# Performance work log

Hardware: AMD Instinct MI355X
Metric: run time of the kernel (lower is better)

The kernel has to match this reference:

```python
import jax, jax.numpy as jnp
from jax import lax
import numpy as np

D_MODEL = 256
EXPAND = 2
D_INNER = D_MODEL * EXPAND
B, T = 8, 4096


def setup_inputs() -> dict:
    key = jax.random.key(0)
    ks = jax.random.split(key, 7)
    s_lin = 1.0 / np.sqrt(D_MODEL)
    s_gru_i = 1.0 / np.sqrt(D_MODEL)  # torch GRU init: U(-1/sqrt(hidden), 1/sqrt(hidden))
    x = jax.random.normal(ks[0], (B, T, D_MODEL), dtype=jnp.float32)
    W1 = jax.random.uniform(ks[1], (D_INNER, D_MODEL), jnp.float32, -s_lin, s_lin)
    b1 = jax.random.uniform(ks[2], (D_INNER,), jnp.float32, -s_lin, s_lin)
    W_ih = jax.random.uniform(ks[3], (3 * D_MODEL, D_INNER), jnp.float32, -s_gru_i, s_gru_i)
    b_ih = jax.random.uniform(ks[4], (3 * D_MODEL,), jnp.float32, -s_gru_i, s_gru_i)
    W_hh = jax.random.uniform(ks[5], (3 * D_MODEL, D_MODEL), jnp.float32, -s_gru_i, s_gru_i)
    b_hh = jax.random.uniform(ks[6], (3 * D_MODEL,), jnp.float32, -s_gru_i, s_gru_i)
    return {"x": x, "W1": W1, "b1": b1, "W_ih": W_ih, "b_ih": b_ih, "W_hh": W_hh, "b_hh": b_hh}


def reference(x, W1, b1, W_ih, b_ih, W_hh, b_hh):
    # Linear(d_model -> d_inner) + exact GELU (torch default)
    h = jax.nn.gelu(jnp.einsum('btd,id->bti', x, W1) + b1, approximate=False)  # [B,T,Di]
    Bb, Tt, _ = h.shape
    H = W_hh.shape[1]
    # Precompute input-side gate pre-activations for all timesteps (order: r, z, n)
    gx = jnp.einsum('bti,gi->btg', h, W_ih) + b_ih  # [B,T,3H]
    gx = jnp.moveaxis(gx, 1, 0)                     # [T,B,3H]

    def step(hprev, g):
        gh = hprev @ W_hh.T + b_hh                  # [B,3H]
        xr, xz, xn = jnp.split(g, 3, axis=-1)
        hr, hz, hn = jnp.split(gh, 3, axis=-1)
        r = jax.nn.sigmoid(xr + hr)
        z = jax.nn.sigmoid(xz + hz)
        n = jnp.tanh(xn + r * hn)
        hnew = (1.0 - z) * n + z * hprev
        return hnew, hnew

    h0 = jnp.zeros((Bb, H), dtype=x.dtype)
    _, out = lax.scan(step, h0, gx)                 # out: [T,B,H]
    return jnp.moveaxis(out, 0, 1)                  # [B,T,H]
```

## Files before the change

### kernel.cpp

```cpp
#include <hip/hip_runtime.h>
#include <hip/hip_fp16.h>
#include <hip/hip_bf16.h>

#define DM   256
#define DI   512
#define TG   768
#define TSEQ 4096
#define NB   8
#define MTOT (NB*TSEQ)

typedef _Float16 h2f __attribute__((ext_vector_type(2)));
typedef _Float16 h8f __attribute__((ext_vector_type(8)));

template<bool A_HALF, bool GELU_ACT>
__global__ __launch_bounds__(256) void gemm_bias(
    const void* __restrict__ Ap, const float* __restrict__ W,
    const float* __restrict__ bias, __half* __restrict__ C,
    int M, int N, int K)
{
  __shared__ float As[16][132];
  __shared__ float Ws[16][132];
  const int tid = threadIdx.x;
  const int tx = tid & 15, ty = tid >> 4;
  const int m0 = blockIdx.y * 128;
  const int n0 = blockIdx.x * 128;

  float acc[8][8] = {};

  for (int k0 = 0; k0 < K; k0 += 16) {
    if constexpr (A_HALF) {
      const __half* A = (const __half*)Ap;
      int r = tid >> 1, seg = (tid & 1) * 8;
      float4 raw = *(const float4*)(A + (size_t)(m0 + r) * K + k0 + seg);
      const __half* hv = (const __half*)&raw;
      #pragma unroll
      for (int q = 0; q < 8; q++) As[seg + q][r] = __half2float(hv[q]);
    } else {
      const float* A = (const float*)Ap;
      #pragma unroll
      for (int rep = 0; rep < 2; rep++) {
        int r = (tid >> 2) + rep * 64;
        int seg = (tid & 3) * 4;
        float4 v = *(const float4*)(A + (size_t)(m0 + r) * K + k0 + seg);
        As[seg + 0][r] = v.x; As[seg + 1][r] = v.y;
        As[seg + 2][r] = v.z; As[seg + 3][r] = v.w;
      }
    }
    #pragma unroll
    for (int rep = 0; rep < 2; rep++) {
      int r = (tid >> 2) + rep * 64;
      int seg = (tid & 3) * 4;
      float4 v = *(const float4*)(W + (size_t)(n0 + r) * K + k0 + seg);
      Ws[seg + 0][r] = v.x; Ws[seg + 1][r] = v.y;
      Ws[seg + 2][r] = v.z; Ws[seg + 3][r] = v.w;
    }
    __syncthreads();
    #pragma unroll
    for (int kk = 0; kk < 16; ++kk) {
      float a[8], b[8];
      *(float4*)&a[0] = *(const float4*)&As[kk][ty * 8];
      *(float4*)&a[4] = *(const float4*)&As[kk][ty * 8 + 4];
      *(float4*)&b[0] = *(const float4*)&Ws[kk][tx * 8];
      *(float4*)&b[4] = *(const float4*)&Ws[kk][tx * 8 + 4];
      #pragma unroll
      for (int i = 0; i < 8; i++)
        #pragma unroll
        for (int j = 0; j < 8; j++)
          acc[i][j] += a[i] * b[j];
    }
    __syncthreads();
  }

  #pragma unroll
  for (int i = 0; i < 8; i++) {
    int m = m0 + ty * 8 + i;
    #pragma unroll
    for (int j = 0; j < 8; j++) {
      int n = n0 + tx * 8 + j;
      float v = acc[i][j] + bias[n];
      if constexpr (GELU_ACT) {
        v = 0.5f * v * (1.0f + erff(v * 0.70710678118654752f));
      }
      C[(size_t)m * N + n] = __float2half(v);
    }
  }
}

__device__ __forceinline__ float dpp_xor1_add(float v) {
  int i = __builtin_bit_cast(int, v);
  int s = __builtin_amdgcn_update_dpp(i, i, 0xB1, 0xF, 0xF, true);
  return v + __builtin_bit_cast(float, s);
}

__global__ __launch_bounds__(512, 2) void gru_scan(
    const __half* __restrict__ gx,
    const float*  __restrict__ Whh,
    const float*  __restrict__ bhh,
    float* __restrict__ out)
{
  const int b = blockIdx.x;
  const int j = threadIdx.x;
  const int u = j >> 1;
  const int p = j & 1;

  __shared__ __align__(16) _Float16 hbuf[2][DM];

  h2f wr[64], wz[64], wn[64];
  {
    const float* rr = Whh + (size_t)u * DM + p * 128;
    const float* rz = rr + (size_t)DM * DM;
    const float* rn = rz + (size_t)DM * DM;
    #pragma unroll
    for (int i = 0; i < 32; ++i) {
      float4 f = *(const float4*)(rr + 4 * i);
      h2f t0; t0[0] = (_Float16)f.x; t0[1] = (_Float16)f.y;
      h2f t1; t1[0] = (_Float16)f.z; t1[1] = (_Float16)f.w;
      wr[2 * i] = t0; wr[2 * i + 1] = t1;
      if (i & 1) __builtin_amdgcn_sched_barrier(0);
    }
    #pragma unroll
    for (int i = 0; i < 32; ++i) {
      float4 f = *(const float4*)(rz + 4 * i);
      h2f t0; t0[0] = (_Float16)f.x; t0[1] = (_Float16)f.y;
      h2f t1; t1[0] = (_Float16)f.z; t1[1] = (_Float16)f.w;
      wz[2 * i] = t0; wz[2 * i + 1] = t1;
      if (i & 1) __builtin_amdgcn_sched_barrier(0);
    }
    #pragma unroll
    for (int i = 0; i < 32; ++i) {
      float4 f = *(const float4*)(rn + 4 * i);
      h2f t0; t0[0] = (_Float16)f.x; t0[1] = (_Float16)f.y;
      h2f t1; t1[0] = (_Float16)f.z; t1[1] = (_Float16)f.w;
      wn[2 * i] = t0; wn[2 * i + 1] = t1;
      if (i & 1) __builtin_amdgcn_sched_barrier(0);
    }
  }
  const float br = bhh[u];
  const float bz = bhh[DM + u];
  const float bn = bhh[2 * DM + u];
  float hloc = 0.0f;

  if (j < DM) hbuf[0][j] = (_Float16)0.0f;
  __syncthreads();

  const __half* gp = gx + (size_t)b * TSEQ * TG;
  float* outb = out + (size_t)b * TSEQ * DM;

  float gxr = __half2float(gp[u]);
  float gxz = __half2float(gp[DM + u]);
  float gxn = __half2float(gp[2 * DM + u]);

  for (int t = 0; t < TSEQ; ++t) {
    const int cur = t & 1;
    const h8f* hp = (const h8f*)(&hbuf[cur][0]) + p * 16;

    float nr = 0.f, nz = 0.f, nn = 0.f;
    if (t + 1 < TSEQ) {
      const __half* g1 = gp + TG;
      nr = __half2float(g1[u]);
      nz = __half2float(g1[DM + u]);
      nn = __half2float(g1[2 * DM + u]);
    }

    float ar = 0.f, az = 0.f, an = 0.f;
    #pragma unroll
    for (int i = 0; i < 16; ++i) {
      union { h8f v; h2f c[4]; } hh;
      hh.v = hp[i];
      ar = __builtin_amdgcn_fdot2(wr[4 * i + 0], hh.c[0], ar, false);
      az = __builtin_amdgcn_fdot2(wz[4 * i + 0], hh.c[0], az, false);
      an = __builtin_amdgcn_fdot2(wn[4 * i + 0], hh.c[0], an, false);
      ar = __builtin_amdgcn_fdot2(wr[4 * i + 1], hh.c[1], ar, false);
      az = __builtin_amdgcn_fdot2(wz[4 * i + 1], hh.c[1], az, false);
      an = __builtin_amdgcn_fdot2(wn[4 * i + 1], hh.c[1], an, false);
      ar = __builtin_amdgcn_fdot2(wr[4 * i + 2], hh.c[2], ar, false);
      az = __builtin_amdgcn_fdot2(wz[4 * i + 2], hh.c[2], az, false);
      an = __builtin_amdgcn_fdot2(wn[4 * i + 2], hh.c[2], an, false);
      ar = __builtin_amdgcn_fdot2(wr[4 * i + 3], hh.c[3], ar, false);
      az = __builtin_amdgcn_fdot2(wz[4 * i + 3], hh.c[3], az, false);
      an = __builtin_amdgcn_fdot2(wn[4 * i + 3], hh.c[3], an, false);
      if (i & 1) __builtin_amdgcn_sched_barrier(0);
    }
    ar = dpp_xor1_add(ar);
    az = dpp_xor1_add(az);
    an = dpp_xor1_add(an);

    float r = 1.0f / (1.0f + __expf(-(gxr + ar + br)));
    float z = 1.0f / (1.0f + __expf(-(gxz + az + bz)));
    float n = tanhf(gxn + r * (an + bn));
    float hnew = (1.0f - z) * n + z * hloc;
    hloc = hnew;

    if (p == 0) {
      hbuf[cur ^ 1][u] = (_Float16)hnew;
      outb[(size_t)t * DM + u] = hnew;
    }
    __syncthreads();

    gp += TG;
    gxr = nr; gxz = nz; gxn = nn;
  }
}

extern "C" void kernel_launch(void* const* d_in, const int* in_sizes, int n_in,
                              void* d_out, int out_size, void* d_ws, size_t ws_size,
                              hipStream_t stream) {
  const float* x   = (const float*)d_in[0];
  const float* W1  = (const float*)d_in[1];
  const float* b1  = (const float*)d_in[2];
  const float* Wih = (const float*)d_in[3];
  const float* bih = (const float*)d_in[4];
  const float* Whh = (const float*)d_in[5];
  const float* bhh = (const float*)d_in[6];
  float* out = (float*)d_out;

  char* ws = (char*)d_ws;
  __half* h  = (__half*)ws;
  size_t h_bytes = (size_t)MTOT * DI * sizeof(__half);
  h_bytes = (h_bytes + 255) & ~(size_t)255;
  __half* gxbuf = (__half*)(ws + h_bytes);

  dim3 blk(256);
  gemm_bias<false, true><<<dim3(DI / 128, MTOT / 128), blk, 0, stream>>>(
      x, W1, b1, h, MTOT, DI, DM);
  gemm_bias<true, false><<<dim3(TG / 128, MTOT / 128), blk, 0, stream>>>(
      h, Wih, bih, gxbuf, MTOT, TG, DI);
  gru_scan<<<NB, 512, 0, stream>>>(gxbuf, Whh, bhh, out);
}
```

Before: 5.879 ms.

## Tune GRU scan: padded h buffer, split accumulators, fast activations, occupancy hint

Several micro-optimizations land together in the serial GRU scan kernel. The shared hidden-state buffer is padded per half so the two lane groups read from separate banks. The dot-product chains are split into two accumulators with software-prefetched LDS loads to shorten dependency chains. Sigmoid and tanh now use hardware reciprocal and a single-exp tanh, and the update is rewritten in fused form. Launch bounds change to min 1 block with an explicit waves-per-EU attribute, which alters register allocation and accepts slightly lower activation accuracy in exchange.

```diff
diff --git a/kernel.cpp b/kernel.cpp
--- a/kernel.cpp
+++ b/kernel.cpp
@@ -92,7 +92,8 @@
   return v + __builtin_bit_cast(float, s);
 }
 
-__global__ __launch_bounds__(512, 2) void gru_scan(
+__global__ __launch_bounds__(512, 1) __attribute__((amdgpu_waves_per_eu(2, 2)))
+void gru_scan(
     const __half* __restrict__ gx,
     const float*  __restrict__ Whh,
     const float*  __restrict__ bhh,
@@ -103,7 +104,7 @@
   const int u = j >> 1;
   const int p = j & 1;
 
-  __shared__ __align__(16) _Float16 hbuf[2][DM];
+  __shared__ __align__(16) _Float16 hbuf[2][2][136];
 
   h2f wr[64], wz[64], wn[64];
   {
@@ -140,7 +141,7 @@
   const float bn = bhh[2 * DM + u];
   float hloc = 0.0f;
 
-  if (j < DM) hbuf[0][j] = (_Float16)0.0f;
+  if (j < DM) hbuf[0][j >> 7][j & 127] = (_Float16)0.0f;
   __syncthreads();
 
   const __half* gp = gx + (size_t)b * TSEQ * TG;
@@ -150,9 +151,28 @@
   float gxz = __half2float(gp[DM + u]);
   float gxn = __half2float(gp[2 * DM + u]);
 
+  #define DOT8(vv, B) do {                                         \
+    h2f c0 = __builtin_shufflevector(vv, vv, 0, 1);                \
+    h2f c1 = __builtin_shufflevector(vv, vv, 2, 3);                \
+    h2f c2 = __builtin_shufflevector(vv, vv, 4, 5);                \
+    h2f c3 = __builtin_shufflevector(vv, vv, 6, 7);                \
+    ar0 = __builtin_amdgcn_fdot2(wr[(B)+0], c0, ar0, false);       \
+    az0 = __builtin_amdgcn_fdot2(wz[(B)+0], c0, az0, false);       \
+    an0 = __builtin_amdgcn_fdot2(wn[(B)+0], c0, an0, false);       \
+    ar1 = __builtin_amdgcn_fdot2(wr[(B)+1], c1, ar1, false);       \
+    az1 = __builtin_amdgcn_fdot2(wz[(B)+1], c1, az1, false);       \
+    an1 = __builtin_amdgcn_fdot2(wn[(B)+1], c1, an1, false);       \
+    ar0 = __builtin_amdgcn_fdot2(wr[(B)+2], c2, ar0, false);       \
+    az0 = __builtin_amdgcn_fdot2(wz[(B)+2], c2, az0, false);       \
+    an0 = __builtin_amdgcn_fdot2(wn[(B)+2], c2, an0, false);       \
+    ar1 = __builtin_amdgcn_fdot2(wr[(B)+3], c3, ar1, false);       \
+    az1 = __builtin_amdgcn_fdot2(wz[(B)+3], c3, az1, false);       \
+    an1 = __builtin_amdgcn_fdot2(wn[(B)+3], c3, an1, false);       \
+  } while (0)
+
   for (int t = 0; t < TSEQ; ++t) {
     const int cur = t & 1;
-    const h8f* hp = (const h8f*)(&hbuf[cur][0]) + p * 16;
+    const h8f* hp = (const h8f*)(&hbuf[cur][p][0]);
 
     float nr = 0.f, nz = 0.f, nn = 0.f;
     if (t + 1 < TSEQ) {
@@ -162,37 +182,29 @@
       nn = __half2float(g1[2 * DM + u]);
     }
 
-    float ar = 0.f, az = 0.f, an = 0.f;
-    #pragma unroll
-    for (int i = 0; i < 16; ++i) {
-      union { h8f v; h2f c[4]; } hh;
-      hh.v = hp[i];
-      ar = __builtin_amdgcn_fdot2(wr[4 * i + 0], hh.c[0], ar, false);
-      az = __builtin_amdgcn_fdot2(wz[4 * i + 0], hh.c[0], az, false);
-      an = __builtin_amdgcn_fdot2(wn[4 * i + 0], hh.c[0], an, false);
-      ar = __builtin_amdgcn_fdot2(wr[4 * i + 1], hh.c[1], ar, false);
-      az = __builtin_amdgcn_fdot2(wz[4 * i + 1], hh.c[1], az, false);
-      an = __builtin_amdgcn_fdot2(wn[4 * i + 1], hh.c[1], an, false);
-      ar = __builtin_amdgcn_fdot2(wr[4 * i + 2], hh.c[2], ar, false);
-      az = __builtin_amdgcn_fdot2(wz[4 * i + 2], hh.c[2], az, false);
-      an = __builtin_amdgcn_fdot2(wn[4 * i + 2], hh.c[2], an, false);
-      ar = __builtin_amdgcn_fdot2(wr[4 * i + 3], hh.c[3], ar, false);
-      az = __builtin_amdgcn_fdot2(wz[4 * i + 3], hh.c[3], az, false);
-      an = __builtin_amdgcn_fdot2(wn[4 * i + 3], hh.c[3], an, false);
-      if (i & 1) __builtin_amdgcn_sched_barrier(0);
-    }
-    ar = dpp_xor1_add(ar);
-    az = dpp_xor1_add(az);
-    an = dpp_xor1_add(an);
-
-    float r = 1.0f / (1.0f + __expf(-(gxr + ar + br)));
-    float z = 1.0f / (1.0f + __expf(-(gxz + az + bz)));
-    float n = tanhf(gxn + r * (an + bn));
-    float hnew = (1.0f - z) * n + z * hloc;
+    float ar0 = 0.f, ar1 = 0.f, az0 = 0.f, az1 = 0.f, an0 = 0.f, an1 = 0.f;
+    h8f v0 = hp[0], v1;
+    #pragma unroll
+    for (int i = 0; i < 16; i += 2) {
+      v1 = hp[i + 1];
+      DOT8(v0, 4 * i);
+      if (i + 2 < 16) v0 = hp[i + 2];
+      DOT8(v1, 4 * i + 4);
+    }
+    float ar = dpp_xor1_add(ar0 + ar1);
+    float az = dpp_xor1_add(az0 + az1);
+    float an = dpp_xor1_add(an0 + an1);
+
+    float r = __builtin_amdgcn_rcpf(1.0f + __expf(-(gxr + ar + br)));
+    float z = __builtin_amdgcn_rcpf(1.0f + __expf(-(gxz + az + bz)));
+    float a = gxn + r * (an + bn);
+    float e = __expf(-2.0f * __builtin_fabsf(a));
+    float n = __builtin_copysignf((1.0f - e) * __builtin_amdgcn_rcpf(1.0f + e), a);
+    float hnew = n + z * (hloc - n);
     hloc = hnew;
 
     if (p == 0) {
-      hbuf[cur ^ 1][u] = (_Float16)hnew;
+      hbuf[cur ^ 1][u >> 7][u & 127] = (_Float16)hnew;
       outb[(size_t)t * DM + u] = hnew;
     }
     __syncthreads();
@@ -200,6 +212,7 @@
     gp += TG;
     gxr = nr; gxz = nz; gxn = nn;
   }
+  #undef DOT8
 }
 
 extern "C" void kernel_launch(void* const* d_in, const int* in_sizes, int n_in,
```

After: 4.945 ms. 15.9% less time.
